# Kernel tuning notes

Hardware: AMD Instinct MI355X
Metric: run time of the kernel (lower is better)

## Reference

```python
import jax, jax.numpy as jnp
import numpy as np

B, T = 1024, 320
EEG_CH, GEO_CH, F1, HID, OUT = 64, 18, 8, 32, 4
THETA0, BETA, TAU_A = 0.5, 1.8, 0.36
EPS = 1e-5


def _bn(x, s, b, m, v):
    # eval-mode BatchNorm with running stats (flax default eps 1e-5)
    return (x - m) * jax.lax.rsqrt(v + EPS) * s + b


def _dwconv(x, w, b, groups):
    # depthwise temporal conv, x: (B, T, C), w: (K, 1, C*F1), SAME padding
    y = jax.lax.conv_general_dilated(x, w, (1,), 'SAME', dimension_numbers=('NWC', 'WIO', 'NWC'), feature_group_count=groups)
    return y + b


def _spike(x):
    return jnp.where(x >= 0.0, 1.0, 0.0)


def _forward(x_eeg, x_geo, eeg_conv_w, eeg_conv_b, eeg_bn1_s, eeg_bn1_b, eeg_bn1_m, eeg_bn1_v, eeg_dense_w, eeg_dense_b, eeg_bn2_s, eeg_bn2_b, eeg_bn2_m, eeg_bn2_v, geo_conv_w, geo_conv_b, geo_bn1_s, geo_bn1_b, geo_bn1_m, geo_bn1_v, geo_dense_w, geo_dense_b, geo_bn2_s, geo_bn2_b, geo_bn2_m, geo_bn2_v, gamma, fc1_w, fc1_b, fc2_w, fc2_b):
    Bc = x_eeg.shape[0]
    xe = _bn(_dwconv(x_eeg, eeg_conv_w, eeg_conv_b, EEG_CH), eeg_bn1_s, eeg_bn1_b, eeg_bn1_m, eeg_bn1_v)
    xe = _bn(xe @ eeg_dense_w + eeg_dense_b, eeg_bn2_s, eeg_bn2_b, eeg_bn2_m, eeg_bn2_v)
    eeg_enc = jax.nn.relu(xe)                      # (B, T, HID)
    xg = _bn(_dwconv(x_geo, geo_conv_w, geo_conv_b, GEO_CH), geo_bn1_s, geo_bn1_b, geo_bn1_m, geo_bn1_v)
    xg = _bn(xg @ geo_dense_w + geo_dense_b, geo_bn2_s, geo_bn2_b, geo_bn2_m, geo_bn2_v)
    geo_mod = jax.nn.sigmoid(xg)                   # (B, T, HID)

    def step(carry, inp):
        m1, m2, m3, ma, eta, mli, prev = carry
        ce, cg = inp
        m1 = 0.9 * m1 + ce; s1 = _spike(m1 - 0.7); m1 = m1 * (1.0 - s1)
        m2 = 0.8 * m2 + ce; s2 = _spike(m2 - 0.5); m2 = m2 * (1.0 - s2)
        m3 = 0.6 * m3 + ce; s3 = _spike(m3 - 0.3); m3 = m3 * (1.0 - s3)
        hr = (s1 + s2 + s3) / 3.0
        eta = TAU_A * eta + (1.0 - TAU_A) * prev
        theta = THETA0 + BETA * eta - gamma * cg
        ma = 0.8 * ma + hr
        sa = _spike(ma - theta)
        ma = ma * (1.0 - sa)
        mli = 0.9 * mli + sa
        return (m1, m2, m3, ma, eta, mli, sa), mli

    z = jnp.zeros((Bc, HID), x_eeg.dtype)
    _, seq = jax.lax.scan(step, (z, z, z, z, z, z, z), (jnp.swapaxes(eeg_enc, 0, 1), jnp.swapaxes(geo_mod, 0, 1)))
    seq = jnp.transpose(seq, (1, 2, 0))            # (B, HID, T)
    win = seq.reshape(Bc, HID, 10, 32)
    dp = (jnp.mean(win[..., 16:], -1) - jnp.mean(win[..., :16], -1)).reshape(Bc, HID * 10)
    return jax.nn.elu(dp @ fc1_w + fc1_b) @ fc2_w + fc2_b


def setup_inputs() -> dict:
    ks = iter(jax.random.split(jax.random.key(0), 48))
    def rn(shape, s=1.0):
        return jax.random.normal(next(ks), shape, jnp.float32) * s
    ECH, GCH = EEG_CH * F1, GEO_CH * F1
    return {
        'x_eeg': rn((B, T, EEG_CH)),
        'x_geo': rn((B, T, GEO_CH)),
        'eeg_conv_w': rn((32, 1, ECH), 0.05), 'eeg_conv_b': jnp.zeros((ECH,), jnp.float32),
        'eeg_bn1_s': 1.0 + rn((ECH,), 0.1), 'eeg_bn1_b': rn((ECH,), 0.1),
        'eeg_bn1_m': rn((ECH,), 0.1), 'eeg_bn1_v': 1.0 + 0.1 * jax.random.uniform(next(ks), (ECH,), jnp.float32),
        'eeg_dense_w': rn((ECH, HID), 0.05), 'eeg_dense_b': jnp.zeros((HID,), jnp.float32),
        'eeg_bn2_s': 1.0 + rn((HID,), 0.1), 'eeg_bn2_b': rn((HID,), 0.1),
        'eeg_bn2_m': rn((HID,), 0.1), 'eeg_bn2_v': 1.0 + 0.1 * jax.random.uniform(next(ks), (HID,), jnp.float32),
        'geo_conv_w': rn((32, 1, GCH), 0.05), 'geo_conv_b': jnp.zeros((GCH,), jnp.float32),
        'geo_bn1_s': 1.0 + rn((GCH,), 0.1), 'geo_bn1_b': rn((GCH,), 0.1),
        'geo_bn1_m': rn((GCH,), 0.1), 'geo_bn1_v': 1.0 + 0.1 * jax.random.uniform(next(ks), (GCH,), jnp.float32),
        'geo_dense_w': rn((GCH, HID), 0.05), 'geo_dense_b': jnp.zeros((HID,), jnp.float32),
        'geo_bn2_s': 1.0 + rn((HID,), 0.1), 'geo_bn2_b': rn((HID,), 0.1),
        'geo_bn2_m': rn((HID,), 0.1), 'geo_bn2_v': 1.0 + 0.1 * jax.random.uniform(next(ks), (HID,), jnp.float32),
        'gamma': jnp.full((HID,), 0.5, jnp.float32),
        'fc1_w': rn((HID * 10, 128), 0.05), 'fc1_b': jnp.zeros((128,), jnp.float32),
        'fc2_w': rn((128, OUT), 0.05), 'fc2_b': jnp.zeros((OUT,), jnp.float32),
    }


def reference(x_eeg, x_geo, eeg_conv_w, eeg_conv_b, eeg_bn1_s, eeg_bn1_b, eeg_bn1_m, eeg_bn1_v, eeg_dense_w, eeg_dense_b, eeg_bn2_s, eeg_bn2_b, eeg_bn2_m, eeg_bn2_v, geo_conv_w, geo_conv_b, geo_bn1_s, geo_bn1_b, geo_bn1_m, geo_bn1_v, geo_dense_w, geo_dense_b, geo_bn2_s, geo_bn2_b, geo_bn2_m, geo_bn2_v, gamma, fc1_w, fc1_b, fc2_w, fc2_b):
    return _forward(x_eeg, x_geo, eeg_conv_w, eeg_conv_b, eeg_bn1_s, eeg_bn1_b, eeg_bn1_m, eeg_bn1_v, eeg_dense_w, eeg_dense_b, eeg_bn2_s, eeg_bn2_b, eeg_bn2_m, eeg_bn2_v, geo_conv_w, geo_conv_b, geo_bn1_s, geo_bn1_b, geo_bn1_m, geo_bn1_v, geo_dense_w, geo_dense_b, geo_bn2_s, geo_bn2_b, geo_bn2_m, geo_bn2_v, gamma, fc1_w, fc1_b, fc2_w, fc2_b)
```

## Files before the change

### kernel.cpp

```cpp
#include <hip/hip_runtime.h>
#include <hip/hip_bf16.h>
#include <math.h>

#define BSZ   1024
#define TLEN  320
#define EEGC  64
#define GEOC  18
#define ECH   512
#define GCH   144
#define HID   32
#define KW    32
#define TT    32
#define NT    (TLEN/TT)
#define BPB   2

#define OFF_ENC  0
#define OFF_MOD  (OFF_ENC + BSZ*TLEN*HID)
#define OFF_DP   (OFF_MOD + BSZ*TLEN*HID)
#define OFF_CWE  (OFF_DP + BSZ*HID*10)
#define OFF_CWG  (OFF_CWE + ECH*KW)
#define OFF_DWE  (OFF_CWG + GCH*KW)
#define OFF_DWG  (OFF_DWE + ECH*HID)
#define OFF_BTE  (OFF_DWG + GCH*HID)
#define OFF_BTG  (OFF_BTE + HID)
#define OFF_GAM  (OFF_BTG + HID)

struct P29 { const float* p[29]; };

__global__ __launch_bounds__(256) void prep_kernel(P29 P, float* __restrict__ ws)
{
    __shared__ float pse[8][32];
    __shared__ float psg[8][32];
    const int tid = threadIdx.x;
    const int gid = blockIdx.x * 256 + tid;
    const int gstride = 33 * 256;
    float* convW_e = ws + OFF_CWE;
    float* convW_g = ws + OFF_CWG;
    float* dW_e    = ws + OFF_DWE;
    float* dW_g    = ws + OFF_DWG;

    for (int i = gid; i < ECH * KW; i += gstride) {
        int c = i >> 5, k = i & 31;
        float A1 = P.p[2][c] * rsqrtf(P.p[5][c] + 1e-5f);
        convW_e[c * KW + k] = P.p[0][(size_t)k * ECH + c] * A1;
    }
    for (int i = gid; i < GCH * KW; i += gstride) {
        int c = i >> 5, k = i & 31;
        float A1 = P.p[14][c] * rsqrtf(P.p[17][c] + 1e-5f);
        convW_g[c * KW + k] = P.p[12][(size_t)k * GCH + c] * A1;
    }
    for (int i = gid; i < ECH * HID; i += gstride) {
        int h = i & 31;
        float A2 = P.p[8][h] * rsqrtf(P.p[11][h] + 1e-5f);
        dW_e[i] = P.p[6][i] * A2;
    }
    for (int i = gid; i < GCH * HID; i += gstride) {
        int h = i & 31;
        float A2 = P.p[20][h] * rsqrtf(P.p[23][h] + 1e-5f);
        dW_g[i] = P.p[18][i] * A2;
    }
    for (int i = gid; i < HID; i += gstride) ws[OFF_GAM + i] = P.p[24][i];

    if (blockIdx.x == 0) {
        {
            const int h = tid & 31, part = tid >> 5;
            float s = 0.f;
            for (int c = part * 64; c < part * 64 + 64; ++c) {
                float A1 = P.p[2][c] * rsqrtf(P.p[5][c] + 1e-5f);
                float C1 = (P.p[1][c] - P.p[4][c]) * A1 + P.p[3][c];
                s += C1 * P.p[6][(size_t)c * HID + h];
            }
            pse[part][h] = s;
            float sg = 0.f;
            for (int c = part * 18; c < part * 18 + 18; ++c) {
                float A1 = P.p[14][c] * rsqrtf(P.p[17][c] + 1e-5f);
                float C1 = (P.p[13][c] - P.p[16][c]) * A1 + P.p[15][c];
                sg += C1 * P.p[18][(size_t)c * HID + h];
            }
            psg[part][h] = sg;
        }
        __syncthreads();
        if (tid < HID) {
            int h = tid;
            float A2 = P.p[8][h] * rsqrtf(P.p[11][h] + 1e-5f);
            float s = pse[0][h] + pse[1][h] + pse[2][h] + pse[3][h]
                    + pse[4][h] + pse[5][h] + pse[6][h] + pse[7][h];
            ws[OFF_BTE + h] = A2 * (s + P.p[7][h] - P.p[10][h]) + P.p[9][h];
        } else if (tid >= 64 && tid < 64 + HID) {
            int h = tid - 64;
            float A2 = P.p[20][h] * rsqrtf(P.p[23][h] + 1e-5f);
            float s = psg[0][h] + psg[1][h] + psg[2][h] + psg[3][h]
                    + psg[4][h] + psg[5][h] + psg[6][h] + psg[7][h];
            ws[OFF_BTG + h] = A2 * (s + P.p[19][h] - P.p[22][h]) + P.p[21][h];
        }
    }
}

__device__ __forceinline__ void conv_stream(const float4* __restrict__ xp4,
                                            const float* __restrict__ w,
                                            float* __restrict__ acc)
{
    float4 cur = xp4[0];
    #pragma unroll
    for (int j4 = 0; j4 < 12; ++j4) {
        float4 nxt = (j4 < 11) ? xp4[j4 + 1] : cur;
        #pragma unroll
        for (int i2 = 0; i2 < 4; ++i2) {
            const int i = j4 * 4 + i2;
            const float xv = (i2 == 0) ? cur.x : (i2 == 1) ? cur.y
                           : (i2 == 2) ? cur.z : cur.w;
            const int tlo = (i - 31 > 0) ? (i - 31) : 0;
            const int thi = (i < 15) ? i : 15;
            #pragma unroll
            for (int t = tlo; t <= thi; ++t)
                acc[t] = fmaf(xv, w[i - t], acc[t]);
        }
        cur = nxt;
    }
}

__device__ __forceinline__ void geo_conv_unit(const float* __restrict__ convW,
                                              const float* __restrict__ xsT,
                                              float* __restrict__ cz,
                                              int c, int th)
{
    float w[KW];
    const float4* wp4 = (const float4*)(convW + c * KW);
    #pragma unroll
    for (int k4 = 0; k4 < 8; ++k4) {
        float4 v = wp4[k4];
        w[4*k4+0]=v.x; w[4*k4+1]=v.y; w[4*k4+2]=v.z; w[4*k4+3]=v.w;
    }
    float acc[16];
    #pragma unroll
    for (int t = 0; t < 16; ++t) acc[t] = 0.f;
    conv_stream((const float4*)(xsT + (c >> 3) * 68 + th * 16), w, acc);
    float4* czp = (float4*)(cz + c * 36 + th * 16);
    czp[0] = make_float4(acc[0],  acc[1],  acc[2],  acc[3]);
    czp[1] = make_float4(acc[4],  acc[5],  acc[6],  acc[7]);
    czp[2] = make_float4(acc[8],  acc[9],  acc[10], acc[11]);
    czp[3] = make_float4(acc[12], acc[13], acc[14], acc[15]);
}

__global__ __launch_bounds__(256)
void path_both(const float* __restrict__ xe, const float* __restrict__ xg,
               float* __restrict__ ws)
{
    __shared__ __align__(16) float smem[6408];

    const int by  = blockIdx.y;
    const int tid = threadIdx.x;

    if (blockIdx.x < NT) {
        const int t0 = blockIdx.x * TT;
        float* xsT = smem;
        float* cz  = smem + 1088;
        const float* convW = ws + OFF_CWE;
        const float* dW    = ws + OFF_DWE;
        float* enc         = ws + OFF_ENC;

        const int tg = tid & 7, hg = (tid >> 3) & 7, q = tid >> 6;
        const int c_loc = tid & 127, th = tid >> 7;

        #pragma unroll 1
        for (int bb = 0; bb < BPB; ++bb) {
            const int b = by * BPB + bb;
            const float* xb = xe + (size_t)b * (TLEN * EEGC);

            float a00=0,a01=0,a02=0,a03=0, a10=0,a11=0,a12=0,a13=0;
            float a20=0,a21=0,a22=0,a23=0, a30=0,a31=0,a32=0,a33=0;

            #pragma unroll 1
            for (int ph = 0; ph < 4; ++ph) {
                if (ph) __syncthreads();
                if (tid < 252) {
                    const int sj = tid >> 2, sc4 = tid & 3;
                    const int st = t0 - 15 + sj;
                    float4 sv = make_float4(0.f, 0.f, 0.f, 0.f);
                    if (st >= 0 && st < TLEN)
                        sv = *(const float4*)(xb + (size_t)st * EEGC + ph * 16 + sc4 * 4);
                    float* p = &xsT[(sc4 * 4) * 68 + sj];
                    p[0] = sv.x; p[68] = sv.y; p[136] = sv.z; p[204] = sv.w;
                }
                __syncthreads();
                {
                    const int c   = ph * 128 + c_loc;
                    const int chl = c_loc >> 3;
                    float w[KW];
                    const float4* wp4 = (const float4*)(convW + c * KW);
                    #pragma unroll
                    for (int k4 = 0; k4 < 8; ++k4) {
                        float4 v = wp4[k4];
                        w[4*k4+0]=v.x; w[4*k4+1]=v.y; w[4*k4+2]=v.z; w[4*k4+3]=v.w;
                    }
                    float acc[16];
                    #pragma unroll
                    for (int t = 0; t < 16; ++t) acc[t] = 0.f;
                    conv_stream((const float4*)(&xsT[chl * 68 + th * 16]), w, acc);
                    float4* czp = (float4*)(cz + c_loc * 36 + th * 16);
                    czp[0] = make_float4(acc[0],  acc[1],  acc[2],  acc[3]);
                    czp[1] = make_float4(acc[4],  acc[5],  acc[6],  acc[7]);
                    czp[2] = make_float4(acc[8],  acc[9],  acc[10], acc[11]);
                    czp[3] = make_float4(acc[12], acc[13], acc[14], acc[15]);
                }
                __syncthreads();
                {
                    const float* dWh = dW + (size_t)(ph * 128 + q * 32) * HID + hg * 4;
                    const float* czb = cz + (q * 32) * 36 + tg * 4;
                    float4 wvb[4], cvb[2];
                    wvb[0] = *(const float4*)(dWh + 0 * HID);
                    wvb[1] = *(const float4*)(dWh + 1 * HID);
                    wvb[2] = *(const float4*)(dWh + 2 * HID);
                    wvb[3] = *(const float4*)(dWh + 3 * HID);
                    cvb[0] = *(const float4*)(czb + 0 * 36);
                    cvb[1] = *(const float4*)(czb + 1 * 36);
                    #pragma unroll
                    for (int ci = 0; ci < 32; ++ci) {
                        float4 cv = cvb[ci & 1];
                        float4 wv = wvb[ci & 3];
                        if (ci + 2 < 32) cvb[ci & 1] = *(const float4*)(czb + (ci + 2) * 36);
                        if (ci + 4 < 32) wvb[ci & 3] = *(const float4*)(dWh + (ci + 4) * HID);
                        a00 = fmaf(cv.x, wv.x, a00); a01 = fmaf(cv.x, wv.y, a01);
                        a02 = fmaf(cv.x, wv.z, a02); a03 = fmaf(cv.x, wv.w, a03);
                        a10 = fmaf(cv.y, wv.x, a10); a11 = fmaf(cv.y, wv.y, a11);
                        a12 = fmaf(cv.y, wv.z, a12); a13 = fmaf(cv.y, wv.w, a13);
                        a20 = fmaf(cv.z, wv.x, a20); a21 = fmaf(cv.z, wv.y, a21);
                        a22 = fmaf(cv.z, wv.z, a22); a23 = fmaf(cv.z, wv.w, a23);
                        a30 = fmaf(cv.w, wv.x, a30); a31 = fmaf(cv.w, wv.y, a31);
                        a32 = fmaf(cv.w, wv.z, a32); a33 = fmaf(cv.w, wv.w, a33);
                    }
                }
            }

            __syncthreads();
            float* stash = cz;
            {
                const int s = (tid >> 1) & 3;
                float4* sp = (float4*)(stash + tid * 16);
                sp[s ^ 0] = make_float4(a00,a01,a02,a03);
                sp[s ^ 1] = make_float4(a10,a11,a12,a13);
                sp[s ^ 2] = make_float4(a20,a21,a22,a23);
                sp[s ^ 3] = make_float4(a30,a31,a32,a33);
            }
            __syncthreads();
            {
                const int t = tid >> 3, hq = tid & 7;
                const int pg = (t & 3) ^ (t >> 3);
                float4 v = make_float4(0.f,0.f,0.f,0.f);
                #pragma unroll
                for (int qq = 0; qq < 4; ++qq) {
                    const int partner = qq * 64 + hq * 8 + (t >> 2);
                    float4 s = *(const float4*)(stash + partner * 16 + pg * 4);
                    v.x += s.x; v.y += s.y; v.z += s.z; v.w += s.w;
                }
                float4 bias = *(const float4*)(ws + OFF_BTE + hq * 4);
                v.x = fmaxf(v.x + bias.x, 0.f);
                v.y = fmaxf(v.y + bias.y, 0.f);
                v.z = fmaxf(v.z + bias.z, 0.f);
                v.w = fmaxf(v.w + bias.w, 0.f);
                *(float4*)(enc + ((size_t)(b * TLEN + t0 + t)) * HID + hq * 4) = v;
            }
        }
    } else {
        const int t0 = (blockIdx.x - NT) * TT;
        float* xsT = smem;
        float* cz  = smem + 1224;
        const float* convW = ws + OFF_CWG;
        const float* dW    = ws + OFF_DWG;
        float* mod         = ws + OFF_MOD;

        const int tg = tid & 7, hg = (tid >> 3) & 7, q = tid >> 6;

        #pragma unroll 1
        for (int bb = 0; bb < BPB; ++bb) {
            const int b = by * BPB + bb;
            const float* xb = xg + (size_t)b * (TLEN * GEOC);

            if (bb) __syncthreads();
            for (int i = tid; i < 63 * GEOC; i += 256) {
                int j = i / GEOC, ch = i - j * GEOC;
                int t = t0 - 15 + j;
                xsT[ch * 68 + j] = (t >= 0 && t < TLEN) ? xb[(size_t)t * GEOC + ch] : 0.f;
            }
            __syncthreads();

            geo_conv_unit(convW, xsT, cz, tid >> 1, tid & 1);
            if (tid < 32)
                geo_conv_unit(convW, xsT, cz, 128 + (tid >> 1), tid & 1);
            __syncthreads();

            float a00=0,a01=0,a02=0,a03=0, a10=0,a11=0,a12=0,a13=0;
            float a20=0,a21=0,a22=0,a23=0, a30=0,a31=0,a32=0,a33=0;
            {
                const float* dWh = dW + (size_t)(q * 36) * HID + hg * 4;
                const float* czb = cz + (q * 36) * 36 + tg * 4;
                #pragma unroll 2
                for (int ci = 0; ci < 36; ++ci) {
                    float4 cv = *(const float4*)(czb + ci * 36);
                    float4 wv = *(const float4*)(dWh + ci * HID);
                    a00 = fmaf(cv.x, wv.x, a00); a01 = fmaf(cv.x, wv.y, a01);
                    a02 = fmaf(cv.x, wv.z, a02); a03 = fmaf(cv.x, wv.w, a03);
                    a10 = fmaf(cv.y, wv.x, a10); a11 = fmaf(cv.y, wv.y, a11);
                    a12 = fmaf(cv.y, wv.z, a12); a13 = fmaf(cv.y, wv.w, a13);
                    a20 = fmaf(cv.z, wv.x, a20); a21 = fmaf(cv.z, wv.y, a21);
                    a22 = fmaf(cv.z, wv.z, a22); a23 = fmaf(cv.z, wv.w, a23);
                    a30 = fmaf(cv.w, wv.x, a30); a31 = fmaf(cv.w, wv.y, a31);
                    a32 = fmaf(cv.w, wv.z, a32); a33 = fmaf(cv.w, wv.w, a33);
                }
            }
            __syncthreads();
            float* stash = cz;
            {
                float4* sp = (float4*)(stash + tid * 20);
                sp[0] = make_float4(a00,a01,a02,a03);
                sp[1] = make_float4(a10,a11,a12,a13);
                sp[2] = make_float4(a20,a21,a22,a23);
                sp[3] = make_float4(a30,a31,a32,a33);
            }
            __syncthreads();
            {
                const int t = tid >> 3, hq = tid & 7;
                float4 v = make_float4(0.f,0.f,0.f,0.f);
                #pragma unroll
                for (int qq = 0; qq < 4; ++qq) {
                    const int partner = qq * 64 + hq * 8 + (t >> 2);
                    float4 s = *(const float4*)(stash + partner * 20 + (t & 3) * 4);
                    v.x += s.x; v.y += s.y; v.z += s.z; v.w += s.w;
                }
                float4 bias = *(const float4*)(ws + OFF_BTG + hq * 4);
                v.x = 1.f / (1.f + expf(-(v.x + bias.x)));
                v.y = 1.f / (1.f + expf(-(v.y + bias.y)));
                v.z = 1.f / (1.f + expf(-(v.z + bias.z)));
                v.w = 1.f / (1.f + expf(-(v.w + bias.w)));
                *(float4*)(mod + ((size_t)(b * TLEN + t0 + t)) * HID + hq * 4) = v;
            }
        }
    }
}

#define SSTEP(CE, CG) { \
    const float ce = (CE), cg = (CG); \
    m1 = 0.9f * m1 + ce; float s1 = ((m1 - 0.7f) >= 0.f) ? 1.f : 0.f; m1 = m1 * (1.f - s1); \
    m2 = 0.8f * m2 + ce; float s2 = ((m2 - 0.5f) >= 0.f) ? 1.f : 0.f; m2 = m2 * (1.f - s2); \
    m3 = 0.6f * m3 + ce; float s3 = ((m3 - 0.3f) >= 0.f) ? 1.f : 0.f; m3 = m3 * (1.f - s3); \
    const float hr = (s1 + s2 + s3) / 3.0f; \
    eta = 0.36f * eta + 0.64f * prev; \
    const float theta = 0.5f + 1.8f * eta - g * cg; \
    ma = 0.8f * ma + hr; \
    const float sa = ((ma - theta) >= 0.f) ? 1.f : 0.f; \
    ma = ma * (1.f - sa); \
    mli = 0.9f * mli + sa; \
    prev = sa; }

__global__ __launch_bounds__(128) void scan_head_kernel(
    float* __restrict__ ws,
    const float* __restrict__ f1w, const float* __restrict__ f1b,
    const float* __restrict__ f2w, const float* __restrict__ f2b,
    float* __restrict__ out)
{
    __shared__ __align__(16) float dps[4][320];
    __shared__ float act[4][128];
    const int tid = threadIdx.x;
    const int grp = tid >> 5, h = tid & 31;
    const int b = blockIdx.x * 4 + grp;

    {
        const float g = ws[OFF_GAM + h];
        const float* pe = ws + OFF_ENC + (size_t)b * TLEN * HID + h;
        const float* pg = ws + OFF_MOD + (size_t)b * TLEN * HID + h;
        float* dpp = &dps[grp][h * 10];

        float m1 = 0.f, m2 = 0.f, m3 = 0.f, ma = 0.f, eta = 0.f, mli = 0.f, prev = 0.f;
        float acc_lo = 0.f, acc_hi = 0.f;
        float ceA[16], cgA[16], ceB[16], cgB[16];

        #pragma unroll
        for (int i = 0; i < 16; ++i) { ceA[i] = pe[i * HID]; cgA[i] = pg[i * HID]; }

        #pragma unroll 1
        for (int ch = 0; ch < 20; ch += 2) {
            const int baseB = (ch + 1) * 16;
            #pragma unroll
            for (int i = 0; i < 16; ++i) {
                ceB[i] = pe[(baseB + i) * HID];
                cgB[i] = pg[(baseB + i) * HID];
            }
            #pragma unroll
            for (int i = 0; i < 16; ++i) {
                SSTEP(ceA[i], cgA[i]);
                acc_lo += mli;
            }
            if (ch + 2 < 20) {
                const int baseA = (ch + 2) * 16;
                #pragma unroll
                for (int i = 0; i < 16; ++i) {
                    ceA[i] = pe[(baseA + i) * HID];
                    cgA[i] = pg[(baseA + i) * HID];
                }
            }
            #pragma unroll
            for (int i = 0; i < 16; ++i) {
                SSTEP(ceB[i], cgB[i]);
                acc_hi += mli;
            }
            dpp[ch >> 1] = acc_hi * (1.f / 16.f) - acc_lo * (1.f / 16.f);
            acc_lo = 0.f; acc_hi = 0.f;
        }
    }
    __syncthreads();

    {
        const int j = tid;
        #pragma unroll 1
        for (int gb = 0; gb < 4; ++gb) {
            const float* dpb = dps[gb];
            float a0 = 0.f, a1 = 0.f, a2 = 0.f, a3 = 0.f;
            #pragma unroll 4
            for (int i = 0; i < 320; i += 4) {
                a0 = fmaf(dpb[i + 0], f1w[(i + 0) * 128 + j], a0);
                a1 = fmaf(dpb[i + 1], f1w[(i + 1) * 128 + j], a1);
                a2 = fmaf(dpb[i + 2], f1w[(i + 2) * 128 + j], a2);
                a3 = fmaf(dpb[i + 3], f1w[(i + 3) * 128 + j], a3);
            }
            float a = f1b[j] + ((a0 + a1) + (a2 + a3));
            act[gb][j] = (a > 0.f) ? a : expm1f(a);
        }
    }
    __syncthreads();

    if (tid < 16) {
        const int gb = tid >> 2, j = tid & 3;
        float o = f2b[j];
        for (int jj = 0; jj < 128; ++jj)
            o = fmaf(act[gb][jj], f2w[jj * 4 + j], o);
        out[(blockIdx.x * 4 + gb) * 4 + j] = o;
    }
}

extern "C" void kernel_launch(void* const* d_in, const int* in_sizes, int n_in,
                              void* d_out, int out_size, void* d_ws, size_t ws_size,
                              hipStream_t stream)
{
    float* ws = (float*)d_ws;

    P29 P;
    for (int k = 0; k < 29; ++k) P.p[k] = (const float*)d_in[k + 2];
    prep_kernel<<<33, 256, 0, stream>>>(P, ws);

    path_both<<<dim3(2 * NT, BSZ / BPB), 256, 0, stream>>>(
        (const float*)d_in[0], (const float*)d_in[1], ws);

    scan_head_kernel<<<BSZ / 4, 128, 0, stream>>>(
        ws, (const float*)d_in[27], (const float*)d_in[28],
        (const float*)d_in[29], (const float*)d_in[30], (float*)d_out);
}
```

Baseline: 687.2 us.

## Double-buffer EEG input staging with async global-to-LDS loads

Replaces the per-phase transpose staging of EEG input into shared memory with two buffers in time-major layout. The next channel phase is prefetched with global_load_lds on interior tiles and with plain loads on edge tiles, so the load overlaps the current phase's conv. The conv loop now reads the untransposed buffer with a stride of 16 through a new inline sliding-window loop instead of conv_stream. This adds shared memory and a sync at the end of each phase, and the strided LDS reads may cause bank conflicts.

```diff
diff --git a/kernel.cpp b/kernel.cpp
--- a/kernel.cpp
+++ b/kernel.cpp
@@ -26,6 +26,10 @@
 #define OFF_GAM  (OFF_BTG + HID)
 
 struct P29 { const float* p[29]; };
+
+#define GLD16(g, l) __builtin_amdgcn_global_load_lds( \
+    (const __attribute__((address_space(1))) void*)(g), \
+    (__attribute__((address_space(3))) void*)(l), 16, 0, 0)
 
 __global__ __launch_bounds__(256) void prep_kernel(P29 P, float* __restrict__ ws)
 {
@@ -146,21 +150,24 @@
 void path_both(const float* __restrict__ xe, const float* __restrict__ xg,
                float* __restrict__ ws)
 {
-    __shared__ __align__(16) float smem[6408];
+    __shared__ __align__(16) float smem[6624];
 
     const int by  = blockIdx.y;
     const int tid = threadIdx.x;
 
     if (blockIdx.x < NT) {
         const int t0 = blockIdx.x * TT;
-        float* xsT = smem;
-        float* cz  = smem + 1088;
+        const bool edge = (blockIdx.x == 0) || (blockIdx.x == NT - 1);
+        float* bufA = smem;
+        float* bufB = smem + 1008;
+        float* cz   = smem + 2016;
         const float* convW = ws + OFF_CWE;
         const float* dW    = ws + OFF_DWE;
         float* enc         = ws + OFF_ENC;
 
         const int tg = tid & 7, hg = (tid >> 3) & 7, q = tid >> 6;
         const int c_loc = tid & 127, th = tid >> 7;
+        const int lane = tid & 63, wvid = tid >> 6;
 
         #pragma unroll 1
         for (int bb = 0; bb < BPB; ++bb) {
@@ -170,33 +177,74 @@
             float a00=0,a01=0,a02=0,a03=0, a10=0,a11=0,a12=0,a13=0;
             float a20=0,a21=0,a22=0,a23=0, a30=0,a31=0,a32=0,a33=0;
 
+            if (bb) __syncthreads();
+
+            if (tid < 252) {
+                const int j = tid >> 2, c4 = tid & 3;
+                const int t = t0 - 15 + j;
+                float4 sv = make_float4(0.f, 0.f, 0.f, 0.f);
+                if (t >= 0 && t < TLEN)
+                    sv = *(const float4*)(xb + (size_t)t * EEGC + c4 * 4);
+                *(float4*)&bufA[tid * 4] = sv;
+            }
+            __syncthreads();
+
             #pragma unroll 1
             for (int ph = 0; ph < 4; ++ph) {
-                if (ph) __syncthreads();
-                if (tid < 252) {
-                    const int sj = tid >> 2, sc4 = tid & 3;
-                    const int st = t0 - 15 + sj;
-                    float4 sv = make_float4(0.f, 0.f, 0.f, 0.f);
-                    if (st >= 0 && st < TLEN)
-                        sv = *(const float4*)(xb + (size_t)st * EEGC + ph * 16 + sc4 * 4);
-                    float* p = &xsT[(sc4 * 4) * 68 + sj];
-                    p[0] = sv.x; p[68] = sv.y; p[136] = sv.z; p[204] = sv.w;
-                }
-                __syncthreads();
+                float* rbuf = (ph & 1) ? bufB : bufA;
+                float* wbuf = (ph & 1) ? bufA : bufB;
+
+                const int c   = ph * 128 + c_loc;
+                const int chl = c_loc >> 3;
+                float w[KW];
                 {
-                    const int c   = ph * 128 + c_loc;
-                    const int chl = c_loc >> 3;
-                    float w[KW];
                     const float4* wp4 = (const float4*)(convW + c * KW);
                     #pragma unroll
                     for (int k4 = 0; k4 < 8; ++k4) {
                         float4 v = wp4[k4];
                         w[4*k4+0]=v.x; w[4*k4+1]=v.y; w[4*k4+2]=v.z; w[4*k4+3]=v.w;
                     }
+                }
+
+                if (ph < 3) {
+                    if (!edge) {
+                        float* dst = wbuf + wvid * 256;
+                        const int f4 = wvid * 64 + lane;
+                        if (f4 < 252) {
+                            const int j = f4 >> 2, c4 = f4 & 3;
+                            const float* g = xb + (size_t)(t0 - 15 + j) * EEGC
+                                           + (ph + 1) * 16 + c4 * 4;
+                            GLD16(g, dst);
+                        }
+                    } else {
+                        if (tid < 252) {
+                            const int j = tid >> 2, c4 = tid & 3;
+                            const int t = t0 - 15 + j;
+                            float4 sv = make_float4(0.f, 0.f, 0.f, 0.f);
+                            if (t >= 0 && t < TLEN)
+                                sv = *(const float4*)(xb + (size_t)t * EEGC
+                                                      + (ph + 1) * 16 + c4 * 4);
+                            *(float4*)&wbuf[tid * 4] = sv;
+                        }
+                    }
+                }
+
+                {
                     float acc[16];
                     #pragma unroll
                     for (int t = 0; t < 16; ++t) acc[t] = 0.f;
-                    conv_stream((const float4*)(&xsT[chl * 68 + th * 16]), w, acc);
+                    const float* xcol = rbuf + chl;
+                    float cur = xcol[(th * 16) * 16];
+                    #pragma unroll
+                    for (int i = 0; i <= 46; ++i) {
+                        float nxt = (i < 46) ? xcol[(th * 16 + i + 1) * 16] : cur;
+                        const int tlo = (i - 31 > 0) ? (i - 31) : 0;
+                        const int thi = (i < 15) ? i : 15;
+                        #pragma unroll
+                        for (int t = tlo; t <= thi; ++t)
+                            acc[t] = fmaf(cur, w[i - t], acc[t]);
+                        cur = nxt;
+                    }
                     float4* czp = (float4*)(cz + c_loc * 36 + th * 16);
                     czp[0] = make_float4(acc[0],  acc[1],  acc[2],  acc[3]);
                     czp[1] = make_float4(acc[4],  acc[5],  acc[6],  acc[7]);
@@ -204,6 +252,7 @@
                     czp[3] = make_float4(acc[12], acc[13], acc[14], acc[15]);
                 }
                 __syncthreads();
+
                 {
                     const float* dWh = dW + (size_t)(ph * 128 + q * 32) * HID + hg * 4;
                     const float* czb = cz + (q * 32) * 36 + tg * 4;
@@ -230,9 +279,9 @@
                         a32 = fmaf(cv.w, wv.z, a32); a33 = fmaf(cv.w, wv.w, a33);
                     }
                 }
-            }
-
-            __syncthreads();
+                __syncthreads();
+            }
+
             float* stash = cz;
             {
                 const int s = (tid >> 1) & 3;
```

Result: slower. 731.4 us (+6.4%).
